# Optimization experiments

Hardware: AMD Instinct MI355X
Metric: run time of the kernel (lower is better)

Reference implementation:

```python
import jax, jax.numpy as jnp
import numpy as np

N = 20000      # nodes
E = 320000     # edges (avg degree 16)
F_IN = 768
DIMS = [(768, 1536), (1536, 768), (768, 384), (384, 256), (256, 5)]


def setup_inputs() -> dict:
    key = jax.random.key(0)
    ks = jax.random.split(key, 2 + 3 * len(DIMS))
    inp = {
        'x': jax.random.normal(ks[0], (N, F_IN), dtype=jnp.float32),
        'edge_index': jax.random.randint(ks[1], (2, E), 0, N, dtype=jnp.int64),
    }
    for li, (fi, fo) in enumerate(DIMS):
        s = 1.0 / np.sqrt(fi)
        inp[f'Wl{li+1}'] = jax.random.uniform(ks[2 + 3 * li], (fi, fo), jnp.float32, -s, s)
        inp[f'Wr{li+1}'] = jax.random.uniform(ks[3 + 3 * li], (fi, fo), jnp.float32, -s, s)
        inp[f'b{li+1}'] = jax.random.uniform(ks[4 + 3 * li], (fo,), jnp.float32, -s, s)
    return inp


def _sage_conv(x, src, dst, deg_inv, Wl, Wr, b):
    # mean aggregate neighbor features, then linear (mean commutes with linear,
    # matching PyG SAGEConv which aggregates x_j then applies lin_l)
    agg = jax.ops.segment_sum(x[src], dst, num_segments=N) * deg_inv  # [N, F_in]
    return agg @ Wl + x @ Wr + b


def reference(x, edge_index,
              Wl1, Wr1, b1, Wl2, Wr2, b2, Wl3, Wr3, b3,
              Wl4, Wr4, b4, Wl5, Wr5, b5):
    src, dst = edge_index[0], edge_index[1]
    deg = jax.ops.segment_sum(jnp.ones((E,), jnp.float32), dst, num_segments=N)
    deg_inv = (1.0 / jnp.maximum(deg, 1.0))[:, None]  # clamp like PyG mean aggr

    h = jax.nn.relu(_sage_conv(x, src, dst, deg_inv, Wl1, Wr1, b1))
    h = jax.nn.relu(_sage_conv(h, src, dst, deg_inv, Wl2, Wr2, b2))
    h = jax.nn.relu(_sage_conv(h, src, dst, deg_inv, Wl3, Wr3, b3))
    h = jax.nn.relu(_sage_conv(h, src, dst, deg_inv, Wl4, Wr4, b4))  # [N, 256]
    out = _sage_conv(h, src, dst, deg_inv, Wl5, Wr5, b5)             # [N, 5]
    return (h, out)
```

## Files before the change

kernel.cpp:

```cpp
#include <hip/hip_runtime.h>
#include <stdint.h>

typedef __attribute__((ext_vector_type(8))) short short8;
typedef __attribute__((ext_vector_type(4))) float f32x4;

__device__ __forceinline__ float bf2f(unsigned short s) {
  return __uint_as_float(((unsigned)s) << 16);
}
__device__ __forceinline__ unsigned short f2bf(float f) {
  unsigned u = __float_as_uint(f);
  u += 0x7fffu + ((u >> 16) & 1u);
  return (unsigned short)(u >> 16);
}

__global__ void gs_scanA(const int* __restrict__ cnt, int* __restrict__ rp,
                         int* __restrict__ bsum, int n) {
  __shared__ int sm[256];
  const int b = blockIdx.x, t = threadIdx.x;
  const int base = b * 1024 + t * 4;
  int v[4]; int s = 0;
#pragma unroll
  for (int i = 0; i < 4; ++i) { v[i] = (base + i < n) ? cnt[base + i] : 0; s += v[i]; }
  sm[t] = s;
  __syncthreads();
  for (int off = 1; off < 256; off <<= 1) {
    int x = (t >= off) ? sm[t - off] : 0;
    __syncthreads();
    sm[t] += x;
    __syncthreads();
  }
  int run = sm[t] - s;
#pragma unroll
  for (int i = 0; i < 4; ++i) { if (base + i < n) rp[base + i] = run; run += v[i]; }
  if (t == 255) bsum[b] = sm[255];
}

__global__ void gs_scanC(int* __restrict__ rp, int* __restrict__ cur,
                         const int* __restrict__ bsum, int n, int nb) {
  __shared__ int sOff[65];
  const int t = threadIdx.x;
  if (t < 64) {
    int bv = (t < nb) ? bsum[t] : 0;
    int run = bv;
#pragma unroll
    for (int off = 1; off < 64; off <<= 1) {
      int x = __shfl_up(run, off, 64);
      if (t >= off) run += x;
    }
    sOff[t] = run - bv;
    if (t == 63) sOff[64] = run;
  }
  __syncthreads();
  int i = blockIdx.x * 256 + threadIdx.x;
  if (i < n) {
    int v = rp[i] + sOff[i >> 10];
    rp[i] = v;
    cur[i] = v;
  }
  if (i == n) rp[n] = sOff[64];
}

__global__ void gs_fill_csr(const int* __restrict__ src, const int* __restrict__ dst,
                            int* __restrict__ cur, int* __restrict__ col, int E) {
  int e = blockIdx.x * 256 + threadIdx.x;
  if (e < E) {
    int pos = atomicAdd(&cur[dst[e]], 1);
    col[pos] = src[e];
  }
}

struct TP { const float* W; unsigned short* WT; int K, F; };
struct TP8 { TP t[8]; int off[9]; };

__global__ __launch_bounds__(256)
void gs_prep(const float* __restrict__ x, unsigned short* __restrict__ xb, int n4,
             const int* __restrict__ dst, int* __restrict__ cnt, int E,
             TP8 args) {
  __shared__ float tb[32][33];
  const int nConv = (n4 + 255) >> 8;
  const int nDeg = (E + 255) >> 8;
  int bid = blockIdx.x;
  if (bid < nConv) {
    int i = bid * 256 + threadIdx.x;
    if (i < n4) {
      float4 f = ((const float4*)x)[i];
      ushort4 o;
      o.x = f2bf(f.x); o.y = f2bf(f.y); o.z = f2bf(f.z); o.w = f2bf(f.w);
      ((ushort4*)xb)[i] = o;
    }
    return;
  }
  bid -= nConv;
  if (bid < nDeg) {
    int e = bid * 256 + threadIdx.x;
    if (e < E) atomicAdd(&cnt[dst[e]], 1);
    return;
  }
  bid -= nDeg;
  int ti = 7;
#pragma unroll
  for (int i = 7; i >= 1; --i)
    if (bid < args.off[i]) ti = i - 1;
  const TP a = args.t[ti];
  const int rem = bid - args.off[ti];
  const int kb = (a.K + 31) >> 5;
  const int k0 = (rem % kb) * 32, f0 = (rem / kb) * 32;
  const int tx = threadIdx.x & 31, ty = threadIdx.x >> 5;
#pragma unroll
  for (int r = ty; r < 32; r += 8) {
    int k = k0 + r, f = f0 + tx;
    tb[r][tx] = (k < a.K && f < a.F) ? a.W[(size_t)k * a.F + f] : 0.f;
  }
  __syncthreads();
#pragma unroll
  for (int r = ty; r < 32; r += 8) {
    int f = f0 + r, k = k0 + tx;
    if (f < a.F && k < a.K) a.WT[(size_t)f * a.K + k] = f2bf(tb[tx][r]);
  }
}

template<int VW>
__global__ __launch_bounds__(64)
void gs_agg_sliceT(const unsigned short* __restrict__ C, int ldc, int zoff,
                   const int* __restrict__ rp, const int* __restrict__ col,
                   const float* __restrict__ bias,
                   unsigned short* __restrict__ hout, float* __restrict__ fout,
                   int F, int relu) {
  const int v = blockIdx.x;
  const int l = threadIdx.x;
  const int cc = blockIdx.y * (64 * VW) + VW * l;
  const int s0 = rp[v], s1 = rp[v + 1];
  const float inv = 1.0f / (float)max(s1 - s0, 1);
  float a[VW];
#pragma unroll
  for (int q = 0; q < VW; ++q) a[q] = 0.f;

  auto addu = [&](ushort4 u) {
    a[0] += bf2f(u.x); a[1] += bf2f(u.y); a[2] += bf2f(u.z); a[3] += bf2f(u.w);
  };
  auto addu2 = [&](ushort2 u) { a[0] += bf2f(u.x); a[1] += bf2f(u.y); };

  for (int base = s0; base < s1; base += 64) {
    int m = min(s1 - base, 64);
    int myNb = (l < m) ? col[base + l] : 0;
    int j = 0;
    for (; j + 8 <= m; j += 8) {
      int n0 = __shfl(myNb, j, 64), n1 = __shfl(myNb, j + 1, 64);
      int n2 = __shfl(myNb, j + 2, 64), n3 = __shfl(myNb, j + 3, 64);
      int n4_ = __shfl(myNb, j + 4, 64), n5 = __shfl(myNb, j + 5, 64);
      int n6 = __shfl(myNb, j + 6, 64), n7 = __shfl(myNb, j + 7, 64);
      if constexpr (VW == 4) {
        ushort4 u0 = *(const ushort4*)(C + (size_t)n0 * ldc + cc);
        ushort4 u1 = *(const ushort4*)(C + (size_t)n1 * ldc + cc);
        ushort4 u2 = *(const ushort4*)(C + (size_t)n2 * ldc + cc);
        ushort4 u3 = *(const ushort4*)(C + (size_t)n3 * ldc + cc);
        ushort4 u4 = *(const ushort4*)(C + (size_t)n4_ * ldc + cc);
        ushort4 u5 = *(const ushort4*)(C + (size_t)n5 * ldc + cc);
        ushort4 u6 = *(const ushort4*)(C + (size_t)n6 * ldc + cc);
        ushort4 u7 = *(const ushort4*)(C + (size_t)n7 * ldc + cc);
        addu(u0); addu(u1); addu(u2); addu(u3);
        addu(u4); addu(u5); addu(u6); addu(u7);
      } else {
        ushort2 u0 = *(const ushort2*)(C + (size_t)n0 * ldc + cc);
        ushort2 u1 = *(const ushort2*)(C + (size_t)n1 * ldc + cc);
        ushort2 u2 = *(const ushort2*)(C + (size_t)n2 * ldc + cc);
        ushort2 u3 = *(const ushort2*)(C + (size_t)n3 * ldc + cc);
        ushort2 u4 = *(const ushort2*)(C + (size_t)n4_ * ldc + cc);
        ushort2 u5 = *(const ushort2*)(C + (size_t)n5 * ldc + cc);
        ushort2 u6 = *(const ushort2*)(C + (size_t)n6 * ldc + cc);
        ushort2 u7 = *(const ushort2*)(C + (size_t)n7 * ldc + cc);
        addu2(u0); addu2(u1); addu2(u2); addu2(u3);
        addu2(u4); addu2(u5); addu2(u6); addu2(u7);
      }
    }
    for (; j < m; ++j) {
      int nj = __shfl(myNb, j, 64);
      if constexpr (VW == 4) addu(*(const ushort4*)(C + (size_t)nj * ldc + cc));
      else addu2(*(const ushort2*)(C + (size_t)nj * ldc + cc));
    }
  }

  float o[VW];
#pragma unroll
  for (int q = 0; q < VW; ++q) o[q] = a[q] * inv;
  if (zoff >= 0) {
    const unsigned short* p = C + (size_t)v * ldc + zoff + cc;
    if constexpr (VW == 4) {
      ushort4 u = *(const ushort4*)p;
      o[0] += bf2f(u.x); o[1] += bf2f(u.y); o[2] += bf2f(u.z); o[3] += bf2f(u.w);
    } else {
      ushort2 u = *(const ushort2*)p;
      o[0] += bf2f(u.x); o[1] += bf2f(u.y);
    }
  }
  if (bias) {
#pragma unroll
    for (int q = 0; q < VW; ++q) o[q] += bias[cc + q];
  }
  if (relu) {
#pragma unroll
    for (int q = 0; q < VW; ++q) o[q] = fmaxf(o[q], 0.f);
  }
  if (hout) {
    if constexpr (VW == 4) {
      ushort4 u; u.x = f2bf(o[0]); u.y = f2bf(o[1]); u.z = f2bf(o[2]); u.w = f2bf(o[3]);
      *(ushort4*)(hout + (size_t)v * F + cc) = u;
    } else {
      ushort2 u; u.x = f2bf(o[0]); u.y = f2bf(o[1]);
      *(ushort2*)(hout + (size_t)v * F + cc) = u;
    }
  }
  if (fout) {
    if constexpr (VW == 4)
      *(float4*)(fout + (size_t)v * F + cc) = make_float4(o[0], o[1], o[2], o[3]);
    else
      *(float2*)(fout + (size_t)v * F + cc) = make_float2(o[0], o[1]);
  }
}

__global__ __launch_bounds__(256)
void gs_l4fuse(const unsigned short* __restrict__ C4,
               const int* __restrict__ rp, const int* __restrict__ col,
               const float* __restrict__ bias4,
               const float* __restrict__ Wl5, const float* __restrict__ Wr5,
               float* __restrict__ houtF, float* __restrict__ yz, int N) {
  __shared__ float sW[2560];
  const int t = threadIdx.x;
  for (int i = t; i < 2560; i += 256) sW[i] = (i < 1280) ? Wl5[i] : Wr5[i - 1280];
  __syncthreads();
  const int v = blockIdx.x * 4 + (t >> 6);
  if (v >= N) return;
  const int l = t & 63;
  const int cc = 4 * l;
  const int s0 = rp[v], s1 = rp[v + 1];
  const float inv = 1.0f / (float)max(s1 - s0, 1);
  float a[4] = {0.f, 0.f, 0.f, 0.f};
  auto addu = [&](ushort4 u) {
    a[0] += bf2f(u.x); a[1] += bf2f(u.y); a[2] += bf2f(u.z); a[3] += bf2f(u.w);
  };
  for (int base = s0; base < s1; base += 64) {
    int m = min(s1 - base, 64);
    int myNb = (l < m) ? col[base + l] : 0;
    int j = 0;
    for (; j + 8 <= m; j += 8) {
      int n0 = __shfl(myNb, j, 64), n1 = __shfl(myNb, j + 1, 64);
      int n2 = __shfl(myNb, j + 2, 64), n3 = __shfl(myNb, j + 3, 64);
      int n4_ = __shfl(myNb, j + 4, 64), n5 = __shfl(myNb, j + 5, 64);
      int n6 = __shfl(myNb, j + 6, 64), n7 = __shfl(myNb, j + 7, 64);
      ushort4 u0 = *(const ushort4*)(C4 + (size_t)n0 * 512 + cc);
      ushort4 u1 = *(const ushort4*)(C4 + (size_t)n1 * 512 + cc);
      ushort4 u2 = *(const ushort4*)(C4 + (size_t)n2 * 512 + cc);
      ushort4 u3 = *(const ushort4*)(C4 + (size_t)n3 * 512 + cc);
      ushort4 u4 = *(const ushort4*)(C4 + (size_t)n4_ * 512 + cc);
      ushort4 u5 = *(const ushort4*)(C4 + (size_t)n5 * 512 + cc);
      ushort4 u6 = *(const ushort4*)(C4 + (size_t)n6 * 512 + cc);
      ushort4 u7 = *(const ushort4*)(C4 + (size_t)n7 * 512 + cc);
      addu(u0); addu(u1); addu(u2); addu(u3);
      addu(u4); addu(u5); addu(u6); addu(u7);
    }
    for (; j < m; ++j) {
      int nj = __shfl(myNb, j, 64);
      addu(*(const ushort4*)(C4 + (size_t)nj * 512 + cc));
    }
  }
  ushort4 us = *(const ushort4*)(C4 + (size_t)v * 512 + 256 + cc);
  float o[4];
  o[0] = fmaxf(a[0] * inv + bf2f(us.x) + bias4[cc + 0], 0.f);
  o[1] = fmaxf(a[1] * inv + bf2f(us.y) + bias4[cc + 1], 0.f);
  o[2] = fmaxf(a[2] * inv + bf2f(us.z) + bias4[cc + 2], 0.f);
  o[3] = fmaxf(a[3] * inv + bf2f(us.w) + bias4[cc + 3], 0.f);
  *(float4*)(houtF + (size_t)v * 256 + cc) = make_float4(o[0], o[1], o[2], o[3]);

  float acc[10];
#pragma unroll
  for (int n = 0; n < 10; ++n) acc[n] = 0.f;
#pragma unroll
  for (int tt = 0; tt < 4; ++tt) {
    int k = cc + tt;
#pragma unroll
    for (int n = 0; n < 5; ++n) {
      acc[n] += o[tt] * sW[k * 5 + n];
      acc[5 + n] += o[tt] * sW[1280 + k * 5 + n];
    }
  }
#pragma unroll
  for (int n = 0; n < 10; ++n)
    for (int off = 32; off > 0; off >>= 1) acc[n] += __shfl_down(acc[n], off, 64);
  if (l == 0) {
#pragma unroll
    for (int n = 0; n < 10; ++n) yz[(size_t)v * 10 + n] = acc[n];
  }
}

#define GLL(SRC, DST) __builtin_amdgcn_global_load_lds(                        \
    (const __attribute__((address_space(1))) unsigned int*)(SRC),              \
    (__attribute__((address_space(3))) unsigned int*)(DST), 16, 0, 0)

#define PHASE(T, MH, NH, RD_A, RD_B, ST_T, ST_B, ST_H, DO_VM)                  \
  {                                                                            \
    const int buf_ = (T) & 1;                                                  \
    if (RD_A) {                                                                \
      const unsigned short* Ab_ = &lA[buf_][MH][0];                            \
      _Pragma("unroll")                                                        \
      for (int fi = 0; fi < 4; ++fi) {                                         \
        int lra = wMl + fi * 16;                                               \
        _Pragma("unroll")                                                      \
        for (int ks = 0; ks < 2; ++ks) {                                       \
          int ch = (ks * 4 + qk) ^ (lra & 7);                                  \
          rA[fi][ks] = *(const short8*)&Ab_[lra * 64 + ch * 8];                \
        }                                                                      \
      }                                                                        \
    }                                                                          \
    if (RD_B) {                                                                \
      const unsigned short* Bb_ = &lB[buf_][NH][0];                            \
      _Pragma("unroll")                                                        \
      for (int fj = 0; fj < 2; ++fj) {                                         \
        int lrb = wNl + fj * 16;                                               \
        _Pragma("unroll")                                                      \
        for (int ks = 0; ks < 2; ++ks) {                                       \
          int ch = (ks * 4 + qk) ^ (lrb & 7);                                  \
          rB[NH][fj][ks] = *(const short8*)&Bb_[lrb * 64 + ch * 8];            \
        }                                                                      \
      }                                                                        \
    }                                                                          \
    STAGE(ST_T, ST_B, ST_H);                                                   \
    __builtin_amdgcn_s_setprio(1);                                             \
    _Pragma("unroll")                                                          \
    for (int fi = 0; fi < 4; ++fi)                                             \
      _Pragma("unroll")                                                        \
      for (int fj = 0; fj < 2; ++fj)                                           \
        _Pragma("unroll")                                                      \
        for (int ks = 0; ks < 2; ++ks)                                         \
          acc[MH][fi][NH][fj] = __builtin_amdgcn_mfma_f32_16x16x32_bf16(       \
              rA[fi][ks], rB[NH][fj][ks], acc[MH][fi][NH][fj], 0, 0, 0);       \
    __builtin_amdgcn_s_setprio(0);                                             \
    if (DO_VM) asm volatile("s_waitcnt vmcnt(4)" ::: "memory");                \
    asm volatile("s_barrier" ::: "memory");                                    \
  }

__global__ __launch_bounds__(512, 2)
void gs_gemm(const unsigned short* __restrict__ A1, const unsigned short* __restrict__ A2,
             const unsigned short* __restrict__ B1, const unsigned short* __restrict__ B2,
             const float* __restrict__ bias, unsigned short* __restrict__ Hout,
             int M, int Nn, int K, int doRelu, int Mt, int Nt) {
  __shared__ unsigned short lA[2][2][8192];
  __shared__ unsigned short lB[2][2][8192];
  const int tid = threadIdx.x;
  const int wid = tid >> 6;
  const int lane = tid & 63;

  const int MG = 8;
  const int per = MG * Nt;
  const int g = blockIdx.x / per;
  const int rem = blockIdx.x - g * per;
  const int gsz = min(MG, Mt - g * MG);
  const int nIdx = rem / gsz;
  const int mIdx = g * MG + (rem - nIdx * gsz);
  const int bM = mIdx * 256;
  const int bN = nIdx * 256;

  const int wM_ = wid >> 2;
  const int wN_ = wid & 3;
  const int qk  = lane >> 4;
  const int wMl = wM_ * 64 + (lane & 15);
  const int wNl = wN_ * 32 + (lane & 15);

  const int lr  = tid >> 3;
  const int swk = ((tid & 7) ^ (lr & 7)) * 8;
  const int rB0 = (lr >> 5) * 64 + (lr & 31);

  const int kt = K / 64;
  const int nt = A2 ? 2 * kt : kt;
  const int NI = nt / 2;

  f32x4 acc[2][4][2][2];
#pragma unroll
  for (int a = 0; a < 2; ++a)
#pragma unroll
    for (int b = 0; b < 4; ++b)
#pragma unroll
      for (int c = 0; c < 2; ++c)
#pragma unroll
        for (int d = 0; d < 2; ++d) acc[a][b][c][d] = (f32x4){0.f, 0.f, 0.f, 0.f};

  short8 rA[4][2];
  short8 rB[2][2][2];

  size_t offA[2][2], offB[2][2];
#pragma unroll
  for (int h = 0; h < 2; ++h) {
    int r1u = bM + h * 64 + lr;
    int r1 = (r1u < M) ? r1u : (M - 1);
    int r2u = r1u + 128;
    int r2 = (r2u < M) ? r2u : (M - 1);
    offA[h][0] = (size_t)r1 * K + swk;
    offA[h][1] = (size_t)r2 * K + swk;
    int rb = bN + h * 32 + rB0;
    offB[h][0] = (size_t)rb * K + swk;
    offB[h][1] = (size_t)(rb + 128) * K + swk;
  }

  auto STAGE = [&](int t, int isB, int h) {
    const int tc = (t < nt) ? t : (nt - 1);
    const int pass = (tc >= kt) ? 1 : 0;
    const int k0 = (tc - pass * kt) * 64;
    const int buf = t & 1;
    if (!isB) {
      const unsigned short* Ap = (pass ? A2 : A1) + k0;
      char* d = (char*)&lA[buf][h][0] + wid * 1024;
      GLL(Ap + offA[h][0], d);
      GLL(Ap + offA[h][1], d + 8192);
    } else {
      const unsigned short* Bp = (pass ? B2 : B1) + k0;
      char* d = (char*)&lB[buf][h][0] + wid * 1024;
      GLL(Bp + offB[h][0], d);
      GLL(Bp + offB[h][1], d + 8192);
    }
  };

  STAGE(0, 0, 0); STAGE(0, 1, 0); STAGE(0, 0, 1); STAGE(0, 1, 1);
  STAGE(1, 0, 0); STAGE(1, 1, 0);
  asm volatile("s_waitcnt vmcnt(4)" ::: "memory");
  asm volatile("s_barrier" ::: "memory");

  for (int i = 0; i < NI; ++i) {
    const int t0 = 2 * i, t1 = t0 + 1, t2 = t0 + 2, t3 = t0 + 3;
    PHASE(t0, 0, 0, 1, 1, t1, 0, 1, 0)
    PHASE(t0, 0, 1, 0, 1, t1, 1, 1, 0)
    PHASE(t0, 1, 0, 1, 0, t2, 0, 0, 0)
    PHASE(t0, 1, 1, 0, 0, t2, 1, 0, 1)
    PHASE(t1, 0, 0, 1, 1, t2, 0, 1, 0)
    PHASE(t1, 0, 1, 0, 1, t2, 1, 1, 0)
    PHASE(t1, 1, 0, 1, 0, t3, 0, 0, 0)
    PHASE(t1, 1, 1, 0, 0, t3, 1, 0, 1)
  }

#pragma unroll
  for (int mh = 0; mh < 2; ++mh)
#pragma unroll
    for (int fi = 0; fi < 4; ++fi) {
      const int row0 = bM + wM_ * 128 + mh * 64 + fi * 16 + (lane >> 4) * 4;
#pragma unroll
      for (int r = 0; r < 4; ++r) {
        const int row = row0 + r;
        if (row >= M) continue;
#pragma unroll
        for (int nh = 0; nh < 2; ++nh)
#pragma unroll
          for (int fj = 0; fj < 2; ++fj) {
            const int colN = bN + wN_ * 64 + nh * 32 + fj * 16 + (lane & 15);
            float v = acc[mh][fi][nh][fj][r];
            if (bias) v += bias[colN];
            if (doRelu) v = fmaxf(v, 0.f);
            Hout[(size_t)row * Nn + colN] = f2bf(v);
          }
      }
    }
}

__global__ __launch_bounds__(256)
void gs_l5agg(const float* __restrict__ yz, const int* __restrict__ rp,
              const int* __restrict__ col, const float* __restrict__ b,
              float* __restrict__ out, int N) {
  const int t = threadIdx.x;
  const int v = blockIdx.x * 16 + (t >> 4);
  if (v >= N) return;
  const int l = t & 15;
  const int s0 = rp[v], s1 = rp[v + 1];
  const float inv = 1.0f / (float)max(s1 - s0, 1);
  float acc[5] = {0.f, 0.f, 0.f, 0.f, 0.f};
  for (int e = s0 + l; e < s1; e += 16) {
    const float* yr = yz + (size_t)col[e] * 10;
#pragma unroll
    for (int n = 0; n < 5; ++n) acc[n] += yr[n];
  }
#pragma unroll
  for (int n = 0; n < 5; ++n) {
    acc[n] += __shfl_down(acc[n], 8, 16);
    acc[n] += __shfl_down(acc[n], 4, 16);
    acc[n] += __shfl_down(acc[n], 2, 16);
    acc[n] += __shfl_down(acc[n], 1, 16);
  }
  if (l == 0) {
#pragma unroll
    for (int n = 0; n < 5; ++n)
      out[(size_t)v * 5 + n] = acc[n] * inv + yz[(size_t)v * 10 + 5 + n] + b[n];
  }
}

extern "C" void kernel_launch(void* const* d_in, const int* in_sizes, int n_in,
                              void* d_out, int out_size, void* d_ws, size_t ws_size,
                              hipStream_t stream) {
  const float* x = (const float*)d_in[0];
  const int* ei = (const int*)d_in[1];
  const int N = in_sizes[0] / 768;
  const int E = in_sizes[1] / 2;
  const int* src = ei;
  const int* dst = ei + E;

  const float* Wl[5];
  const float* Wr[5];
  const float* bb[5];
  for (int l = 0; l < 5; ++l) {
    Wl[l] = (const float*)d_in[2 + 3 * l];
    Wr[l] = (const float*)d_in[3 + 3 * l];
    bb[l] = (const float*)d_in[4 + 3 * l];
  }

  char* w = (char*)d_ws;
  size_t off = 0;
  auto take = [&](size_t bytes) -> char* {
    char* p = w + off;
    off = (off + bytes + 255) & ~(size_t)255;
    return p;
  };
  unsigned short* ar1 = (unsigned short*)take((size_t)N * 768 * 2);
  unsigned short* ar2 = (unsigned short*)take((size_t)N * 768 * 2);
  unsigned short* ar3 = (unsigned short*)take((size_t)N * 1536 * 2);
  unsigned short* C2  = (unsigned short*)take((size_t)N * 1536 * 2);
  int* cnt  = (int*)take((size_t)N * 4);
  int* rp   = (int*)take((size_t)(N + 1) * 4);
  int* cur  = (int*)take((size_t)N * 4);
  int* col  = (int*)take((size_t)E * 4);
  const int nbChunks = (N + 1023) / 1024;
  int* bsum = (int*)take((size_t)(nbChunks + 1) * 4);
  unsigned short* WT1l = (unsigned short*)take((size_t)1536 * 768 * 2);
  unsigned short* WT1r = (unsigned short*)take((size_t)1536 * 768 * 2);
  unsigned short* WT2  = (unsigned short*)take((size_t)1536 * 1536 * 2);
  unsigned short* WT3  = (unsigned short*)take((size_t)768 * 768 * 2);
  unsigned short* WT4  = (unsigned short*)take((size_t)512 * 384 * 2);

  unsigned short* xb   = ar1;
  unsigned short* C3   = ar1;
  unsigned short* aggb = ar2;
  unsigned short* h2   = ar2;
  unsigned short* h1   = ar3;
  unsigned short* C4   = ar3;
  unsigned short* h3   = ar3 + (size_t)N * 512;
  float*          yz5  = (float*)(ar3 + (size_t)N * (512 + 384));

  const int M = N;
  const int Mt = (M + 255) / 256;

  hipMemsetAsync(cnt, 0, (size_t)N * 4, stream);
  TP8 tp;
  tp.t[0] = {Wl[0], WT1l, 768, 1536};
  tp.t[1] = {Wr[0], WT1r, 768, 1536};
  tp.t[2] = {Wl[1], WT2, 1536, 768};
  tp.t[3] = {Wr[1], WT2 + (size_t)768 * 1536, 1536, 768};
  tp.t[4] = {Wl[2], WT3, 768, 384};
  tp.t[5] = {Wr[2], WT3 + (size_t)384 * 768, 768, 384};
  tp.t[6] = {Wl[3], WT4, 384, 256};
  tp.t[7] = {Wr[3], WT4 + (size_t)256 * 384, 384, 256};
  tp.off[0] = 0;
  for (int i = 0; i < 8; ++i) {
    int kb = (tp.t[i].K + 31) >> 5, fb = (tp.t[i].F + 31) >> 5;
    tp.off[i + 1] = tp.off[i] + kb * fb;
  }
  const int n4 = N * 768 / 4;
  const int prepBlocks = ((n4 + 255) >> 8) + ((E + 255) >> 8) + tp.off[8];
  gs_prep<<<prepBlocks, 256, 0, stream>>>(x, xb, n4, dst, cnt, E, tp);

  gs_scanA<<<nbChunks, 256, 0, stream>>>(cnt, rp, bsum, N);
  gs_scanC<<<(N + 256) / 256, 256, 0, stream>>>(rp, cur, bsum, N, nbChunks);
  gs_fill_csr<<<(E + 255) / 256, 256, 0, stream>>>(src, dst, cur, col, E);

  float* houtF = (float*)d_out;
  float* out5  = (float*)d_out + (size_t)N * 256;

  gs_agg_sliceT<4><<<dim3(N, 3), 64, 0, stream>>>(xb, 768, -1, rp, col, nullptr, aggb, nullptr, 768, 0);
  gs_gemm<<<Mt * 6, 512, 0, stream>>>(aggb, xb, WT1l, WT1r, bb[0], h1, M, 1536, 768, 1, Mt, 6);

  gs_gemm<<<Mt * 6, 512, 0, stream>>>(h1, nullptr, WT2, nullptr, nullptr, C2, M, 1536, 1536, 0, Mt, 6);
  gs_agg_sliceT<4><<<dim3(N, 3), 64, 0, stream>>>(C2, 1536, 768, rp, col, bb[1], h2, nullptr, 768, 1);

  gs_gemm<<<Mt * 3, 512, 0, stream>>>(h2, nullptr, WT3, nullptr, nullptr, C3, M, 768, 768, 0, Mt, 3);
  gs_agg_sliceT<2><<<dim3(N, 3), 64, 0, stream>>>(C3, 768, 384, rp, col, bb[2], h3, nullptr, 384, 1);

  gs_gemm<<<Mt * 2, 512, 0, stream>>>(h3, nullptr, WT4, nullptr, nullptr, C4, M, 512, 384, 0, Mt, 2);
  gs_l4fuse<<<(N + 3) / 4, 256, 0, stream>>>(C4, rp, col, bb[3], Wl[4], Wr[4], houtF, yz5, N);

  gs_l5agg<<<(N + 15) / 16, 256, 0, stream>>>(yz5, rp, col, bb[4], out5, N);
}
```

Baseline: 631.5 us.

## Double-buffer LDS fragment registers to overlap reads with MFMA phases

Restructures the GEMM main loop so A and B fragment reads from LDS go into alternating register sets (aX/aY, bX/bY). The next tile's first fragments are prefetched at the end of each iteration, so LDS reads overlap MFMA work instead of stalling at phase starts. Each phase issues its global-to-LDS stage and MFMAs between barriers, and the loop now runs per k-tile instead of in pairs. The extra fragment registers raise register pressure under the 512x2 launch bound and could cause spills.

```diff
diff --git a/kernel.cpp b/kernel.cpp
--- a/kernel.cpp
+++ b/kernel.cpp
@@ -296,34 +296,33 @@
     (const __attribute__((address_space(1))) unsigned int*)(SRC),              \
     (__attribute__((address_space(3))) unsigned int*)(DST), 16, 0, 0)
 
-#define PHASE(T, MH, NH, RD_A, RD_B, ST_T, ST_B, ST_H, DO_VM)                  \
-  {                                                                            \
-    const int buf_ = (T) & 1;                                                  \
-    if (RD_A) {                                                                \
-      const unsigned short* Ab_ = &lA[buf_][MH][0];                            \
+#define RDA(DST, BUF, MH) {                                                    \
+    const unsigned short* Ab_ = &lA[BUF][MH][0];                               \
+    _Pragma("unroll")                                                          \
+    for (int fi = 0; fi < 4; ++fi) {                                           \
+      int lra = wMl + fi * 16;                                                 \
       _Pragma("unroll")                                                        \
-      for (int fi = 0; fi < 4; ++fi) {                                         \
-        int lra = wMl + fi * 16;                                               \
-        _Pragma("unroll")                                                      \
-        for (int ks = 0; ks < 2; ++ks) {                                       \
-          int ch = (ks * 4 + qk) ^ (lra & 7);                                  \
-          rA[fi][ks] = *(const short8*)&Ab_[lra * 64 + ch * 8];                \
-        }                                                                      \
+      for (int ks = 0; ks < 2; ++ks) {                                         \
+        int ch = (ks * 4 + qk) ^ (lra & 7);                                    \
+        DST[fi][ks] = *(const short8*)&Ab_[lra * 64 + ch * 8];                 \
       }                                                                        \
     }                                                                          \
-    if (RD_B) {                                                                \
-      const unsigned short* Bb_ = &lB[buf_][NH][0];                            \
+  }
+
+#define RDB(DST, BUF, NH) {                                                    \
+    const unsigned short* Bb_ = &lB[BUF][NH][0];                               \
+    _Pragma("unroll")                                                          \
+    for (int fj = 0; fj < 2; ++fj) {                                           \
+      int lrb = wNl + fj * 16;                                                 \
       _Pragma("unroll")                                                        \
-      for (int fj = 0; fj < 2; ++fj) {                                         \
-        int lrb = wNl + fj * 16;                                               \
-        _Pragma("unroll")                                                      \
-        for (int ks = 0; ks < 2; ++ks) {                                       \
-          int ch = (ks * 4 + qk) ^ (lrb & 7);                                  \
-          rB[NH][fj][ks] = *(const short8*)&Bb_[lrb * 64 + ch * 8];            \
-        }                                                                      \
+      for (int ks = 0; ks < 2; ++ks) {                                         \
+        int ch = (ks * 4 + qk) ^ (lrb & 7);                                    \
+        DST[fj][ks] = *(const short8*)&Bb_[lrb * 64 + ch * 8];                 \
       }                                                                        \
     }                                                                          \
-    STAGE(ST_T, ST_B, ST_H);                                                   \
+  }
+
+#define MF(MH, FA, NH, FB) {                                                   \
     __builtin_amdgcn_s_setprio(1);                                             \
     _Pragma("unroll")                                                          \
     for (int fi = 0; fi < 4; ++fi)                                             \
@@ -332,11 +331,12 @@
         _Pragma("unroll")                                                      \
         for (int ks = 0; ks < 2; ++ks)                                         \
           acc[MH][fi][NH][fj] = __builtin_amdgcn_mfma_f32_16x16x32_bf16(       \
-              rA[fi][ks], rB[NH][fj][ks], acc[MH][fi][NH][fj], 0, 0, 0);       \
+              FA[fi][ks], FB[fj][ks], acc[MH][fi][NH][fj], 0, 0, 0);           \
     __builtin_amdgcn_s_setprio(0);                                             \
-    if (DO_VM) asm volatile("s_waitcnt vmcnt(4)" ::: "memory");                \
-    asm volatile("s_barrier" ::: "memory");                                    \
-  }
+  }
+
+#define BAR asm volatile("s_barrier" ::: "memory")
+#define VMC4 asm volatile("s_waitcnt vmcnt(4)" ::: "memory")
 
 __global__ __launch_bounds__(512, 2)
 void gs_gemm(const unsigned short* __restrict__ A1, const unsigned short* __restrict__ A2,
@@ -371,7 +371,6 @@
 
   const int kt = K / 64;
   const int nt = A2 ? 2 * kt : kt;
-  const int NI = nt / 2;
 
   f32x4 acc[2][4][2][2];
 #pragma unroll
@@ -383,8 +382,10 @@
 #pragma unroll
         for (int d = 0; d < 2; ++d) acc[a][b][c][d] = (f32x4){0.f, 0.f, 0.f, 0.f};
 
-  short8 rA[4][2];
-  short8 rB[2][2][2];
+  short8 aX[4][2];
+  short8 aY[4][2];
+  short8 bX[2][2];
+  short8 bY[2][2];
 
   size_t offA[2][2], offB[2][2];
 #pragma unroll
@@ -420,19 +421,31 @@
 
   STAGE(0, 0, 0); STAGE(0, 1, 0); STAGE(0, 0, 1); STAGE(0, 1, 1);
   STAGE(1, 0, 0); STAGE(1, 1, 0);
-  asm volatile("s_waitcnt vmcnt(4)" ::: "memory");
-  asm volatile("s_barrier" ::: "memory");
-
-  for (int i = 0; i < NI; ++i) {
-    const int t0 = 2 * i, t1 = t0 + 1, t2 = t0 + 2, t3 = t0 + 3;
-    PHASE(t0, 0, 0, 1, 1, t1, 0, 1, 0)
-    PHASE(t0, 0, 1, 0, 1, t1, 1, 1, 0)
-    PHASE(t0, 1, 0, 1, 0, t2, 0, 0, 0)
-    PHASE(t0, 1, 1, 0, 0, t2, 1, 0, 1)
-    PHASE(t1, 0, 0, 1, 1, t2, 0, 1, 0)
-    PHASE(t1, 0, 1, 0, 1, t2, 1, 1, 0)
-    PHASE(t1, 1, 0, 1, 0, t3, 0, 0, 0)
-    PHASE(t1, 1, 1, 0, 0, t3, 1, 0, 1)
+  VMC4;
+  BAR;
+  RDA(aX, 0, 0)
+  RDB(bX, 0, 0)
+
+  for (int t = 0; t < nt; ++t) {
+    const int cb = t & 1;
+    const int nb2 = cb ^ 1;
+    RDB(bY, cb, 1)
+    STAGE(t + 1, 0, 1);
+    MF(0, aX, 0, bX)
+    BAR;
+    RDA(aY, cb, 1)
+    STAGE(t + 1, 1, 1);
+    MF(0, aX, 1, bY)
+    BAR;
+    STAGE(t + 2, 0, 0);
+    MF(1, aY, 0, bX)
+    BAR;
+    STAGE(t + 2, 1, 0);
+    MF(1, aY, 1, bY)
+    VMC4;
+    BAR;
+    RDA(aX, nb2, 0)
+    RDB(bX, nb2, 0)
   }
 
 #pragma unroll
```

Result: slower. 657.4 us (+4.1%).
